# Kernel optimization log

Measured on AMD Instinct MI355X. Metric: run time of the kernel, lower is better.

## Reference

```python
import jax, jax.numpy as jnp
import numpy as np

B, T, C = 2, 2048, 1024
H = 4 * C           # MLP hidden (4*n_embd)
E_DYN = 7           # num_experts - static_experts
TOP_K = 2           # num_experts_per_tok
MOE_LOSS_COEF = 0.01


def setup_inputs() -> dict:
    key = jax.random.key(0)
    ks = jax.random.split(key, 6)
    s = 0.02
    x = jax.random.normal(ks[0], (B, T, C), dtype=jnp.float32)
    gate_w = jax.random.normal(ks[1], (C, E_DYN), dtype=jnp.float32) * s
    w1 = jax.random.normal(ks[2], (E_DYN, C, H), dtype=jnp.float32) * s   # dynamic experts c_fc
    w2 = jax.random.normal(ks[3], (E_DYN, H, C), dtype=jnp.float32) * s   # dynamic experts c_proj
    w1s = jax.random.normal(ks[4], (C, H), dtype=jnp.float32) * s         # static expert c_fc
    w2s = jax.random.normal(ks[5], (H, C), dtype=jnp.float32) * s         # static expert c_proj
    return {"x": x, "gate_w": gate_w, "w1": w1, "w2": w2, "w1s": w1s, "w2s": w2s}


def reference(x, gate_w, w1, w2, w1s, w2s):
    b, t, c = x.shape
    xf = x.reshape(-1, c)                                   # [N, C]
    n = xf.shape[0]

    # static expert (always applied)
    y_static = jax.nn.gelu(xf @ w1s, approximate=False) @ w2s  # [N, C]

    # gating: top-k + softmax over selected scores
    scores = xf @ gate_w                                    # [N, E]
    topk_scores, topk_idx = jax.lax.top_k(scores, TOP_K)    # [N, K]
    topk_w = jax.nn.softmax(topk_scores, axis=-1)           # [N, K]

    # dense dispatch weights [N, E] (top_k indices are distinct -> set is safe)
    probs = jnp.zeros((n, E_DYN), dtype=x.dtype)
    probs = probs.at[jnp.arange(n)[:, None], topk_idx].set(topk_w)

    # all-expert MLP then weighted combine (same math as masked per-expert dispatch)
    h = jax.nn.gelu(jnp.einsum('nc,ech->enh', xf, w1), approximate=False)  # [E, N, H]
    y_all = jnp.einsum('enh,ehc->enc', h, w2)               # [E, N, C]
    y_dyn = jnp.einsum('ne,enc->nc', probs, y_all)          # [N, C]

    y = (y_dyn + y_static).reshape(b, t, c)

    # variance_penalty auxiliary loss
    expert_usage = probs.mean(axis=0)                       # [E]
    variance = jnp.mean((expert_usage - expert_usage.mean()) ** 2)
    aux = MOE_LOSS_COEF * variance
    return y, aux
```

## Files before the change

kernel.cpp:

```cpp
#include <hip/hip_runtime.h>
#include <hip/hip_bf16.h>
#include <math.h>

#define N_TOK 4096
#define C_DIM 1024
#define H_DIM 4096
#define NEXP 7
#define NGRP 8
#define HCAP 13184

typedef __attribute__((ext_vector_type(8))) short short8;
typedef __attribute__((ext_vector_type(4))) float floatx4;

static const size_t OFF_COUNTS = 0;
static const size_t OFF_CURSOR = 64;
static const size_t OFF_BASE   = 128;
static const size_t OFF_PCOUNT = 192;
static const size_t OFF_CNT8   = 256;
static const size_t OFF_USAGE  = 320;
static const size_t OFF_TOPKI  = 4096;
static const size_t OFF_TOPKW  = OFF_TOPKI + 8192ull * 4;
static const size_t OFF_ETOK   = OFF_TOPKW + 8192ull * 4;
static const size_t OFF_EWT    = OFF_ETOK + (size_t)HCAP * 4;
static const size_t OFF_EIDX   = OFF_EWT + (size_t)HCAP * 4;
static const size_t OFF_XB     = 262144;
static const size_t OFF_W1T    = OFF_XB + (size_t)N_TOK * C_DIM * 2;
static const size_t OFF_W2T    = OFF_W1T + (size_t)NGRP * H_DIM * C_DIM * 2;
static const size_t OFF_H      = OFF_W2T + (size_t)NGRP * C_DIM * H_DIM * 2;

static __device__ __forceinline__ unsigned short f2bf(float f) {
    __hip_bfloat16 b = __float2bfloat16(f);
    return *reinterpret_cast<unsigned short*>(&b);
}
static __device__ __forceinline__ float bf2f(unsigned short u) {
    unsigned int v = ((unsigned int)u) << 16;
    return __builtin_bit_cast(float, v);
}

static __device__ __forceinline__ float gelu_f(float v) {
    float z = v * 0.70710678118654752f;
    float az = fabsf(z);
    float t = 1.0f / (1.0f + 0.3275911f * az);
    float poly = t * (0.254829592f + t * (-0.284496736f + t * (1.421413741f +
                 t * (-1.453152027f + t * 1.061405429f))));
    float erf_abs = 1.0f - poly * __expf(-az * az);
    float erf_v = (z < 0.f) ? -erf_abs : erf_abs;
    return 0.5f * v * (1.0f + erf_v);
}

static __device__ __forceinline__ void gll16(const void* g, void* l) {
    __builtin_amdgcn_global_load_lds((const __attribute__((address_space(1))) void*)g,
                                     (__attribute__((address_space(3))) void*)l, 16, 0, 0);
}

template <int VM> static __device__ __forceinline__ void wait_vm() {
    if constexpr (VM == 8) asm volatile("s_waitcnt vmcnt(8)" ::: "memory");
    else if constexpr (VM == 4) asm volatile("s_waitcnt vmcnt(4)" ::: "memory");
    else asm volatile("s_waitcnt vmcnt(0)" ::: "memory");
}
static __device__ __forceinline__ void barf() {
    __builtin_amdgcn_s_barrier();
    asm volatile("" ::: "memory");
}
static __device__ __forceinline__ void lgkm0_bar() {
    asm volatile("s_waitcnt lgkmcnt(0)" ::: "memory");
    __builtin_amdgcn_s_barrier();
    asm volatile("" ::: "memory");
}

static __device__ __forceinline__ void mfma_step(const char* Ap, const char* Bp,
    int wm, int wn, int l16, int rswz, floatx4 (&acc)[4][4])
{
    short8 a[4], b[4];
#pragma unroll
    for (int i = 0; i < 4; i++) {
        a[i] = *(const short8*)(Ap + ((wm * 64 + i * 16 + l16) * 64 + rswz));
        b[i] = *(const short8*)(Bp + ((wn * 64 + i * 16 + l16) * 64 + rswz));
    }
    __builtin_amdgcn_s_setprio(1);
#pragma unroll
    for (int i = 0; i < 4; i++)
#pragma unroll
        for (int j = 0; j < 4; j++)
            acc[i][j] = __builtin_amdgcn_mfma_f32_16x16x32_bf16(a[i], b[j], acc[i][j], 0, 0, 0);
    __builtin_amdgcn_s_setprio(0);
}

__global__ void init_small_kernel(int* counts, int* cursor, float* usage) {
    int i = threadIdx.x;
    if (i < 8) { counts[i] = 0; cursor[i] = 0; usage[i] = 0.f; }
}

__global__ void convert_x_kernel(const float* __restrict__ x, unsigned short* __restrict__ xb) {
    int i = blockIdx.x * 256 + threadIdx.x;
    float4 v = ((const float4*)x)[i];
    ushort4 o;
    o.x = f2bf(v.x); o.y = f2bf(v.y); o.z = f2bf(v.z); o.w = f2bf(v.w);
    ((ushort4*)xb)[i] = o;
}

__global__ __launch_bounds__(256) void transpose_cvt_kernel(
    const float* __restrict__ dyn, const float* __restrict__ stat,
    __hip_bfloat16* __restrict__ dst, int R, int S)
{
    int e = blockIdx.z;
    const float* src = (e < NEXP) ? (dyn + (size_t)e * R * S) : stat;
    unsigned short* d = (unsigned short*)(dst + (size_t)e * R * S);
    int s0 = blockIdx.x * 32, r0 = blockIdx.y * 64;
    __shared__ float t[64][33];
    int tx4 = threadIdx.x & 15, ty4 = threadIdx.x >> 4;
#pragma unroll
    for (int i = 0; i < 4; i++) {
        int r = ty4 + i * 16;
        float2 v = *(const float2*)(src + (size_t)(r0 + r) * S + s0 + tx4 * 2);
        t[r][tx4 * 2] = v.x; t[r][tx4 * 2 + 1] = v.y;
    }
    __syncthreads();
    int tx3 = threadIdx.x & 31, ty3 = threadIdx.x >> 5;
#pragma unroll
    for (int i = 0; i < 4; i++) {
        int s = ty3 + i * 8;
        int r = tx3 * 2;
        ushort2 o;
        o.x = f2bf(t[r][s]); o.y = f2bf(t[r + 1][s]);
        *(ushort2*)(d + (size_t)(s0 + s) * R + r0 + r) = o;
    }
}

__global__ __launch_bounds__(256) void gate_kernel(
    const float* __restrict__ x, const float* __restrict__ gw,
    int* __restrict__ topki, float* __restrict__ topkw,
    int* counts, float* usage)
{
    int wid = threadIdx.x >> 6, lane = threadIdx.x & 63;
    int t = blockIdx.x * 4 + wid;
    float s[NEXP];
#pragma unroll
    for (int e = 0; e < NEXP; e++) s[e] = 0.f;
    for (int c = lane; c < C_DIM; c += 64) {
        float xv = x[(size_t)t * C_DIM + c];
#pragma unroll
        for (int e = 0; e < NEXP; e++) s[e] += xv * gw[c * NEXP + e];
    }
#pragma unroll
    for (int e = 0; e < NEXP; e++)
        for (int off = 32; off > 0; off >>= 1) s[e] += __shfl_xor(s[e], off);
    if (lane == 0) {
        int e0 = 0;
        for (int e = 1; e < NEXP; e++) if (s[e] > s[e0]) e0 = e;
        int e1 = -1;
        for (int e = 0; e < NEXP; e++) {
            if (e == e0) continue;
            if (e1 < 0 || s[e] > s[e1]) e1 = e;
        }
        float w0 = 1.f / (1.f + expf(s[e1] - s[e0]));
        float w1 = 1.f - w0;
        topki[t * 2] = e0; topki[t * 2 + 1] = e1;
        topkw[t * 2] = w0; topkw[t * 2 + 1] = w1;
        atomicAdd(&counts[e0], 1); atomicAdd(&counts[e1], 1);
        atomicAdd(&usage[e0], w0); atomicAdd(&usage[e1], w1);
    }
}

__global__ __launch_bounds__(256) void prefix_kernel(
    const int* counts, const float* usage,
    int* base, int* pcount, int* cnt8,
    int* etok, float* ewt, float* y, int aux_index)
{
    __shared__ int sb[NGRP], sc[NGRP], sp[NGRP];
    if (threadIdx.x == 0) {
        int run = 0;
        for (int g = 0; g < NEXP; g++) {
            int c = counts[g];
            int p = (c + 127) & ~127;
            base[g] = run; pcount[g] = p; cnt8[g] = c;
            sb[g] = run; sc[g] = c; sp[g] = p;
            run += p;
        }
        base[NEXP] = run; pcount[NEXP] = N_TOK; cnt8[NEXP] = N_TOK;
        sb[NEXP] = run; sc[NEXP] = N_TOK; sp[NEXP] = N_TOK;
        float u[NEXP]; float mean = 0.f;
        for (int e = 0; e < NEXP; e++) { u[e] = usage[e] / (float)N_TOK; mean += u[e]; }
        mean /= (float)NEXP;
        float var = 0.f;
        for (int e = 0; e < NEXP; e++) { float dd = u[e] - mean; var += dd * dd; }
        var /= (float)NEXP;
        y[aux_index] = 0.01f * var;
    }
    __syncthreads();
    for (int i = threadIdx.x; i < N_TOK; i += 256) {
        etok[sb[NEXP] + i] = i; ewt[sb[NEXP] + i] = 1.0f;
    }
    for (int g = 0; g < NEXP; g++) {
        for (int i = sc[g] + (int)threadIdx.x; i < sp[g]; i += 256) {
            etok[sb[g] + i] = 0; ewt[sb[g] + i] = 0.f;
        }
    }
}

__global__ void scatter_kernel(const int* __restrict__ topki, const float* __restrict__ topkw,
                               const int* __restrict__ base, int* cursor,
                               int* __restrict__ etok, float* __restrict__ ewt,
                               int* __restrict__ eidx)
{
    int i = blockIdx.x * 256 + threadIdx.x;
    int t = i >> 1;
    int e = topki[i];
    float w = topkw[i];
    int pos = atomicAdd(&cursor[e], 1);
    int idx = base[e] + pos;
    etok[idx] = t; ewt[idx] = w;
    eidx[i] = idx;
}

__global__ __launch_bounds__(256) void gemm1_kernel(
    const __hip_bfloat16* __restrict__ xb,
    const __hip_bfloat16* __restrict__ w1t,
    __hip_bfloat16* __restrict__ h,
    const int* __restrict__ etok,
    const int* __restrict__ base,
    const int* __restrict__ pcount)
{
    int g = blockIdx.z, mt = blockIdx.y, ct = blockIdx.x;
    if (mt * 128 >= pcount[g]) return;
    int eb = base[g];

    __shared__ __align__(16) char Ab[3][8192];
    __shared__ __align__(16) char Bb[3][8192];

    int tid = threadIdx.x;
    int lane = tid & 63, wid = tid >> 6;
    int quad = lane >> 4, l16 = lane & 15;
    int wm = wid >> 1, wn = wid & 1;
    int rsub = lane >> 2, chunk = lane & 3;
    int swzc = chunk ^ ((rsub >> 1) & 3);
    int rswz = (quad ^ ((l16 >> 1) & 3)) * 16;

    const char* gA[2]; const char* gB[2]; int lo[2];
#pragma unroll
    for (int j = 0; j < 2; j++) {
        int row = wid * 32 + j * 16 + rsub;
        int tok = etok[eb + mt * 128 + row];
        gA[j] = (const char*)(xb + (size_t)tok * C_DIM) + swzc * 16;
        gB[j] = (const char*)(w1t + ((size_t)g * H_DIM + ct * 128 + row) * C_DIM) + swzc * 16;
        lo[j] = (wid * 32 + j * 16) * 64;
    }

#define STG(p, kt) do { size_t so = (size_t)(kt) * 64; \
        gll16(gA[0] + so, Ab[p] + lo[0]); \
        gll16(gA[1] + so, Ab[p] + lo[1]); \
        gll16(gB[0] + so, Bb[p] + lo[0]); \
        gll16(gB[1] + so, Bb[p] + lo[1]); } while (0)

    floatx4 acc[4][4] = {};
    const int nt = C_DIM / 32;
    STG(0, 0); STG(1, 1);
    int p = 0;
    for (int t = 0; t + 2 < nt; ++t) {
        int pn = p + 2; if (pn >= 3) pn -= 3;
        STG(pn, t + 2);
        wait_vm<8>();
        barf();
        mfma_step(Ab[p], Bb[p], wm, wn, l16, rswz, acc);
        lgkm0_bar();
        if (++p == 3) p = 0;
    }
    wait_vm<4>(); barf();
    mfma_step(Ab[0], Bb[0], wm, wn, l16, rswz, acc);
    lgkm0_bar();
    wait_vm<0>(); barf();
    mfma_step(Ab[1], Bb[1], wm, wn, l16, rswz, acc);
#undef STG

#pragma unroll
    for (int i = 0; i < 4; i++) {
        int rbase = mt * 128 + wm * 64 + i * 16 + quad * 4;
#pragma unroll
        for (int reg = 0; reg < 4; reg++) {
            size_t hrow = (size_t)(eb + rbase + reg) * H_DIM;
#pragma unroll
            for (int j = 0; j < 4; j++) {
                int cc = ct * 128 + wn * 64 + j * 16 + l16;
                h[hrow + cc] = __float2bfloat16(gelu_f(acc[i][j][reg]));
            }
        }
    }
}

__global__ __launch_bounds__(256) void gemm2_kernel(
    const __hip_bfloat16* __restrict__ h,
    const __hip_bfloat16* __restrict__ w2t,
    unsigned short* __restrict__ yp,
    const int* __restrict__ base,
    const int* __restrict__ pcount)
{
    int id = blockIdx.x;
    int xcd = id & 7;
    int jj  = id >> 3;
    int ct  = jj & 7;
    int g4  = xcd + ((jj >> 3) << 3);
    int mt  = g4 & 63, g = g4 >> 6;
    if (mt * 128 >= pcount[g]) return;
    int eb = base[g];

    __shared__ __align__(16) char Ab[3][8192];
    __shared__ __align__(16) char Bb[3][8192];

    int tid = threadIdx.x;
    int lane = tid & 63, wid = tid >> 6;
    int quad = lane >> 4, l16 = lane & 15;
    int wm = wid >> 1, wn = wid & 1;
    int rsub = lane >> 2, chunk = lane & 3;
    int swzc = chunk ^ ((rsub >> 1) & 3);
    int rswz = (quad ^ ((l16 >> 1) & 3)) * 16;

    const char* gA[2]; const char* gB[2]; int lo[2];
#pragma unroll
    for (int j = 0; j < 2; j++) {
        int row = wid * 32 + j * 16 + rsub;
        gA[j] = (const char*)(h + (size_t)(eb + mt * 128 + row) * H_DIM) + swzc * 16;
        gB[j] = (const char*)(w2t + ((size_t)g * C_DIM + ct * 128 + row) * H_DIM) + swzc * 16;
        lo[j] = (wid * 32 + j * 16) * 64;
    }

#define STG(p, kt) do { size_t so = (size_t)(kt) * 64; \
        gll16(gA[0] + so, Ab[p] + lo[0]); \
        gll16(gA[1] + so, Ab[p] + lo[1]); \
        gll16(gB[0] + so, Bb[p] + lo[0]); \
        gll16(gB[1] + so, Bb[p] + lo[1]); } while (0)

    floatx4 acc[4][4] = {};
    const int nt = H_DIM / 32;
    STG(0, 0); STG(1, 1);
    int p = 0;
    for (int t = 0; t + 2 < nt; ++t) {
        int pn = p + 2; if (pn >= 3) pn -= 3;
        STG(pn, t + 2);
        wait_vm<8>();
        barf();
        mfma_step(Ab[p], Bb[p], wm, wn, l16, rswz, acc);
        lgkm0_bar();
        if (++p == 3) p = 0;
    }
    wait_vm<4>(); barf();
    mfma_step(Ab[0], Bb[0], wm, wn, l16, rswz, acc);
    lgkm0_bar();
    wait_vm<0>(); barf();
    mfma_step(Ab[1], Bb[1], wm, wn, l16, rswz, acc);
#undef STG

#pragma unroll
    for (int i = 0; i < 4; i++) {
        int rl0 = mt * 128 + wm * 64 + i * 16 + quad * 4;
#pragma unroll
        for (int reg = 0; reg < 4; reg++) {
            size_t yrow = (size_t)(eb + rl0 + reg) * C_DIM;
#pragma unroll
            for (int j = 0; j < 4; j++) {
                int cc = ct * 128 + wn * 64 + j * 16 + l16;
                yp[yrow + cc] = f2bf(acc[i][j][reg]);
            }
        }
    }
}

__global__ __launch_bounds__(256) void combine_kernel(
    const unsigned short* __restrict__ yp,
    const int* __restrict__ eidx,
    const float* __restrict__ topkw,
    const int* __restrict__ base,
    float* __restrict__ y)
{
    int t = blockIdx.x;
    int i0 = eidx[t * 2], i1 = eidx[t * 2 + 1];
    float w0 = topkw[t * 2], w1 = topkw[t * 2 + 1];
    int is = base[NEXP] + t;
    int c = threadIdx.x * 4;
    ushort4 a = *(const ushort4*)(yp + (size_t)i0 * C_DIM + c);
    ushort4 b = *(const ushort4*)(yp + (size_t)i1 * C_DIM + c);
    ushort4 s = *(const ushort4*)(yp + (size_t)is * C_DIM + c);
    float4 o;
    o.x = w0 * bf2f(a.x) + w1 * bf2f(b.x) + bf2f(s.x);
    o.y = w0 * bf2f(a.y) + w1 * bf2f(b.y) + bf2f(s.y);
    o.z = w0 * bf2f(a.z) + w1 * bf2f(b.z) + bf2f(s.z);
    o.w = w0 * bf2f(a.w) + w1 * bf2f(b.w) + bf2f(s.w);
    *(float4*)(y + (size_t)t * C_DIM + c) = o;
}

extern "C" void kernel_launch(void* const* d_in, const int* in_sizes, int n_in,
                              void* d_out, int out_size, void* d_ws, size_t ws_size,
                              hipStream_t stream) {
    const float* x      = (const float*)d_in[0];
    const float* gate_w = (const float*)d_in[1];
    const float* w1     = (const float*)d_in[2];
    const float* w2     = (const float*)d_in[3];
    const float* w1s    = (const float*)d_in[4];
    const float* w2s    = (const float*)d_in[5];
    float* y = (float*)d_out;
    char* ws = (char*)d_ws;

    int*   counts = (int*)(ws + OFF_COUNTS);
    int*   cursor = (int*)(ws + OFF_CURSOR);
    int*   base   = (int*)(ws + OFF_BASE);
    int*   pcount = (int*)(ws + OFF_PCOUNT);
    int*   cnt8   = (int*)(ws + OFF_CNT8);
    float* usage  = (float*)(ws + OFF_USAGE);
    int*   topki  = (int*)(ws + OFF_TOPKI);
    float* topkw  = (float*)(ws + OFF_TOPKW);
    int*   etok   = (int*)(ws + OFF_ETOK);
    float* ewt    = (float*)(ws + OFF_EWT);
    int*   eidx   = (int*)(ws + OFF_EIDX);
    unsigned short* xb_u = (unsigned short*)(ws + OFF_XB);
    __hip_bfloat16* xb  = (__hip_bfloat16*)(ws + OFF_XB);
    __hip_bfloat16* w1t = (__hip_bfloat16*)(ws + OFF_W1T);
    __hip_bfloat16* w2t = (__hip_bfloat16*)(ws + OFF_W2T);
    __hip_bfloat16* hbuf = (__hip_bfloat16*)(ws + OFF_H);
    unsigned short* yp  = (unsigned short*)(ws + OFF_W1T);

    init_small_kernel<<<1, 64, 0, stream>>>(counts, cursor, usage);

    convert_x_kernel<<<(N_TOK * C_DIM / 4) / 256, 256, 0, stream>>>(x, xb_u);
    transpose_cvt_kernel<<<dim3(H_DIM / 32, C_DIM / 64, NGRP), 256, 0, stream>>>(w1, w1s, w1t, C_DIM, H_DIM);
    transpose_cvt_kernel<<<dim3(C_DIM / 32, H_DIM / 64, NGRP), 256, 0, stream>>>(w2, w2s, w2t, H_DIM, C_DIM);

    gate_kernel<<<N_TOK / 4, 256, 0, stream>>>(x, gate_w, topki, topkw, counts, usage);
    prefix_kernel<<<1, 256, 0, stream>>>(counts, usage, base, pcount, cnt8, etok, ewt, y, N_TOK * C_DIM);
    scatter_kernel<<<(N_TOK * 2) / 256, 256, 0, stream>>>(topki, topkw, base, cursor, etok, ewt, eidx);

    gemm1_kernel<<<dim3(H_DIM / 128, 64, NGRP), 256, 0, stream>>>(xb, w1t, hbuf, etok, base, pcount);
    gemm2_kernel<<<4096, 256, 0, stream>>>(hbuf, w2t, yp, base, pcount);
    combine_kernel<<<N_TOK, 256, 0, stream>>>(yp, eidx, topkw, base, y);
}
```

Baseline: 843.6 us.

## Enlarge grouped GEMM tiles to 256x256 with 8 waves and 4-stage LDS pipeline

Both expert GEMM kernels move from 128x128 tiles with 4 waves and triple buffering to 256x256 tiles with 8 waves, each wave computing a 128x64 sub-tile, plus a 4-deep global-to-LDS prefetch ring with a single barrier per K step. Block-to-tile mapping is redone so an XCD's blocks share expert and M-tile data across column tiles, and row guards are added for partial tiles. The aim is higher arithmetic intensity per LDS byte and fewer barriers. The cost is 128KB of LDS per block, more padding waste on per-expert row counts, and high register pressure from 32 accumulators per wave.

```diff
diff --git a/kernel.cpp b/kernel.cpp
--- a/kernel.cpp
+++ b/kernel.cpp
@@ -53,37 +53,12 @@
                                      (__attribute__((address_space(3))) void*)l, 16, 0, 0);
 }
 
-template <int VM> static __device__ __forceinline__ void wait_vm() {
-    if constexpr (VM == 8) asm volatile("s_waitcnt vmcnt(8)" ::: "memory");
-    else if constexpr (VM == 4) asm volatile("s_waitcnt vmcnt(4)" ::: "memory");
-    else asm volatile("s_waitcnt vmcnt(0)" ::: "memory");
-}
+static __device__ __forceinline__ void wait_vm8() { asm volatile("s_waitcnt vmcnt(8)" ::: "memory"); }
+static __device__ __forceinline__ void wait_vm4() { asm volatile("s_waitcnt vmcnt(4)" ::: "memory"); }
+static __device__ __forceinline__ void wait_vm0() { asm volatile("s_waitcnt vmcnt(0)" ::: "memory"); }
 static __device__ __forceinline__ void barf() {
     __builtin_amdgcn_s_barrier();
     asm volatile("" ::: "memory");
-}
-static __device__ __forceinline__ void lgkm0_bar() {
-    asm volatile("s_waitcnt lgkmcnt(0)" ::: "memory");
-    __builtin_amdgcn_s_barrier();
-    asm volatile("" ::: "memory");
-}
-
-static __device__ __forceinline__ void mfma_step(const char* Ap, const char* Bp,
-    int wm, int wn, int l16, int rswz, floatx4 (&acc)[4][4])
-{
-    short8 a[4], b[4];
-#pragma unroll
-    for (int i = 0; i < 4; i++) {
-        a[i] = *(const short8*)(Ap + ((wm * 64 + i * 16 + l16) * 64 + rswz));
-        b[i] = *(const short8*)(Bp + ((wn * 64 + i * 16 + l16) * 64 + rswz));
-    }
-    __builtin_amdgcn_s_setprio(1);
-#pragma unroll
-    for (int i = 0; i < 4; i++)
-#pragma unroll
-        for (int j = 0; j < 4; j++)
-            acc[i][j] = __builtin_amdgcn_mfma_f32_16x16x32_bf16(a[i], b[j], acc[i][j], 0, 0, 0);
-    __builtin_amdgcn_s_setprio(0);
 }
 
 __global__ void init_small_kernel(int* counts, int* cursor, float* usage) {
@@ -213,7 +188,14 @@
     eidx[i] = idx;
 }
 
-__global__ __launch_bounds__(256) void gemm1_kernel(
+
+#define STG1(T) do { int b_ = (T) & 3; size_t so_ = (size_t)(T) * 64; \
+        gll16(pA0 + so_, &Als[b_][w * 1024]); \
+        gll16(pA1 + so_, &Als[b_][8192 + w * 1024]); \
+        gll16(pB0 + so_, &Bls[b_][w * 1024]); \
+        gll16(pB1 + so_, &Bls[b_][8192 + w * 1024]); } while (0)
+
+__global__ __launch_bounds__(512, 2) void gemm1_kernel(
     const __hip_bfloat16* __restrict__ xb,
     const __hip_bfloat16* __restrict__ w1t,
     __hip_bfloat16* __restrict__ h,
@@ -221,73 +203,78 @@
     const int* __restrict__ base,
     const int* __restrict__ pcount)
 {
-    int g = blockIdx.z, mt = blockIdx.y, ct = blockIdx.x;
-    if (mt * 128 >= pcount[g]) return;
+    int id = blockIdx.x;
+    int xcd = id & 7, rest = id >> 3;
+    int ct = rest & 15, s = rest >> 4;
+    int g = s & 7;
+    int mt = ((xcd - g) & 7) + 8 * (s >> 3);
+    int psz = pcount[g];
+    if (mt * 256 >= psz) return;
     int eb = base[g];
 
-    __shared__ __align__(16) char Ab[3][8192];
-    __shared__ __align__(16) char Bb[3][8192];
-
-    int tid = threadIdx.x;
-    int lane = tid & 63, wid = tid >> 6;
+    __shared__ __align__(16) char Als[4][16384];
+    __shared__ __align__(16) char Bls[4][16384];
+
+    int tid = threadIdx.x, lane = tid & 63, w = tid >> 6;
+    int r0 = tid >> 2, c0 = tid & 3;
+    int cs = c0 ^ ((r0 >> 1) & 3);
+
+    int tokA0 = etok[eb + mt * 256 + r0];
+    int tokA1 = etok[eb + mt * 256 + 128 + r0];
+    const char* pA0 = (const char*)(xb + (size_t)tokA0 * C_DIM) + cs * 16;
+    const char* pA1 = (const char*)(xb + (size_t)tokA1 * C_DIM) + cs * 16;
+    const char* pB0 = (const char*)(w1t + ((size_t)g * H_DIM + ct * 256 + r0) * C_DIM) + cs * 16;
+    const char* pB1 = (const char*)(w1t + ((size_t)g * H_DIM + ct * 256 + 128 + r0) * C_DIM) + cs * 16;
+
+    int wm = w >> 2, wn = w & 3;
     int quad = lane >> 4, l16 = lane & 15;
-    int wm = wid >> 1, wn = wid & 1;
-    int rsub = lane >> 2, chunk = lane & 3;
-    int swzc = chunk ^ ((rsub >> 1) & 3);
     int rswz = (quad ^ ((l16 >> 1) & 3)) * 16;
 
-    const char* gA[2]; const char* gB[2]; int lo[2];
-#pragma unroll
-    for (int j = 0; j < 2; j++) {
-        int row = wid * 32 + j * 16 + rsub;
-        int tok = etok[eb + mt * 128 + row];
-        gA[j] = (const char*)(xb + (size_t)tok * C_DIM) + swzc * 16;
-        gB[j] = (const char*)(w1t + ((size_t)g * H_DIM + ct * 128 + row) * C_DIM) + swzc * 16;
-        lo[j] = (wid * 32 + j * 16) * 64;
-    }
-
-#define STG(p, kt) do { size_t so = (size_t)(kt) * 64; \
-        gll16(gA[0] + so, Ab[p] + lo[0]); \
-        gll16(gA[1] + so, Ab[p] + lo[1]); \
-        gll16(gB[0] + so, Bb[p] + lo[0]); \
-        gll16(gB[1] + so, Bb[p] + lo[1]); } while (0)
-
-    floatx4 acc[4][4] = {};
-    const int nt = C_DIM / 32;
-    STG(0, 0); STG(1, 1);
-    int p = 0;
-    for (int t = 0; t + 2 < nt; ++t) {
-        int pn = p + 2; if (pn >= 3) pn -= 3;
-        STG(pn, t + 2);
-        wait_vm<8>();
+    floatx4 acc[8][4] = {};
+    const int NT = C_DIM / 32;
+    STG1(0); STG1(1); STG1(2);
+    for (int T = 0; T < NT; ++T) {
+        int rem = NT - 1 - T;
+        if (rem >= 2) wait_vm8(); else if (rem == 1) wait_vm4(); else wait_vm0();
         barf();
-        mfma_step(Ab[p], Bb[p], wm, wn, l16, rswz, acc);
-        lgkm0_bar();
-        if (++p == 3) p = 0;
-    }
-    wait_vm<4>(); barf();
-    mfma_step(Ab[0], Bb[0], wm, wn, l16, rswz, acc);
-    lgkm0_bar();
-    wait_vm<0>(); barf();
-    mfma_step(Ab[1], Bb[1], wm, wn, l16, rswz, acc);
-#undef STG
-
-#pragma unroll
-    for (int i = 0; i < 4; i++) {
-        int rbase = mt * 128 + wm * 64 + i * 16 + quad * 4;
+        if (T + 3 < NT) STG1(T + 3);
+        const char* Ap = Als[T & 3];
+        const char* Bp = Bls[T & 3];
+        short8 a[8], b[4];
+#pragma unroll
+        for (int i = 0; i < 8; i++)
+            a[i] = *(const short8*)(Ap + (wm * 128 + i * 16 + l16) * 64 + rswz);
+#pragma unroll
+        for (int j = 0; j < 4; j++)
+            b[j] = *(const short8*)(Bp + (wn * 64 + j * 16 + l16) * 64 + rswz);
+        __builtin_amdgcn_s_setprio(1);
+#pragma unroll
+        for (int i = 0; i < 8; i++)
+#pragma unroll
+            for (int j = 0; j < 4; j++)
+                acc[i][j] = __builtin_amdgcn_mfma_f32_16x16x32_bf16(a[i], b[j], acc[i][j], 0, 0, 0);
+        __builtin_amdgcn_s_setprio(0);
+    }
+
+#pragma unroll
+    for (int i = 0; i < 8; i++) {
+        int lr0 = mt * 256 + wm * 128 + i * 16 + quad * 4;
 #pragma unroll
         for (int reg = 0; reg < 4; reg++) {
-            size_t hrow = (size_t)(eb + rbase + reg) * H_DIM;
-#pragma unroll
-            for (int j = 0; j < 4; j++) {
-                int cc = ct * 128 + wn * 64 + j * 16 + l16;
-                h[hrow + cc] = __float2bfloat16(gelu_f(acc[i][j][reg]));
+            int lr = lr0 + reg;
+            if (lr < psz) {
+                size_t hrow = (size_t)(eb + lr) * H_DIM;
+#pragma unroll
+                for (int j = 0; j < 4; j++) {
+                    int cc = ct * 256 + wn * 64 + j * 16 + l16;
+                    h[hrow + cc] = __float2bfloat16(gelu_f(acc[i][j][reg]));
+                }
             }
         }
     }
 }
 
-__global__ __launch_bounds__(256) void gemm2_kernel(
+__global__ __launch_bounds__(512, 2) void gemm2_kernel(
     const __hip_bfloat16* __restrict__ h,
     const __hip_bfloat16* __restrict__ w2t,
     unsigned short* __restrict__ yp,
@@ -295,70 +282,69 @@
     const int* __restrict__ pcount)
 {
     int id = blockIdx.x;
-    int xcd = id & 7;
-    int jj  = id >> 3;
-    int ct  = jj & 7;
-    int g4  = xcd + ((jj >> 3) << 3);
-    int mt  = g4 & 63, g = g4 >> 6;
-    if (mt * 128 >= pcount[g]) return;
+    int xcd = id & 7, rest = id >> 3;
+    int ct = rest & 3, s = rest >> 2;
+    int g = s & 7;
+    int mt = ((xcd - g) & 7) + 8 * (s >> 3);
+    int psz = pcount[g];
+    if (mt * 256 >= psz) return;
     int eb = base[g];
 
-    __shared__ __align__(16) char Ab[3][8192];
-    __shared__ __align__(16) char Bb[3][8192];
-
-    int tid = threadIdx.x;
-    int lane = tid & 63, wid = tid >> 6;
+    __shared__ __align__(16) char Als[4][16384];
+    __shared__ __align__(16) char Bls[4][16384];
+
+    int tid = threadIdx.x, lane = tid & 63, w = tid >> 6;
+    int r0 = tid >> 2, c0 = tid & 3;
+    int cs = c0 ^ ((r0 >> 1) & 3);
+
+    const char* pA0 = (const char*)(h + (size_t)(eb + mt * 256 + r0) * H_DIM) + cs * 16;
+    const char* pA1 = (const char*)(h + (size_t)(eb + mt * 256 + 128 + r0) * H_DIM) + cs * 16;
+    const char* pB0 = (const char*)(w2t + ((size_t)g * C_DIM + ct * 256 + r0) * H_DIM) + cs * 16;
+    const char* pB1 = (const char*)(w2t + ((size_t)g * C_DIM + ct * 256 + 128 + r0) * H_DIM) + cs * 16;
+
+    int wm = w >> 2, wn = w & 3;
     int quad = lane >> 4, l16 = lane & 15;
-    int wm = wid >> 1, wn = wid & 1;
-    int rsub = lane >> 2, chunk = lane & 3;
-    int swzc = chunk ^ ((rsub >> 1) & 3);
     int rswz = (quad ^ ((l16 >> 1) & 3)) * 16;
 
-    const char* gA[2]; const char* gB[2]; int lo[2];
-#pragma unroll
-    for (int j = 0; j < 2; j++) {
-        int row = wid * 32 + j * 16 + rsub;
-        gA[j] = (const char*)(h + (size_t)(eb + mt * 128 + row) * H_DIM) + swzc * 16;
-        gB[j] = (const char*)(w2t + ((size_t)g * C_DIM + ct * 128 + row) * H_DIM) + swzc * 16;
-        lo[j] = (wid * 32 + j * 16) * 64;
-    }
-
-#define STG(p, kt) do { size_t so = (size_t)(kt) * 64; \
-        gll16(gA[0] + so, Ab[p] + lo[0]); \
-        gll16(gA[1] + so, Ab[p] + lo[1]); \
-        gll16(gB[0] + so, Bb[p] + lo[0]); \
-        gll16(gB[1] + so, Bb[p] + lo[1]); } while (0)
-
-    floatx4 acc[4][4] = {};
-    const int nt = H_DIM / 32;
-    STG(0, 0); STG(1, 1);
-    int p = 0;
-    for (int t = 0; t + 2 < nt; ++t) {
-        int pn = p + 2; if (pn >= 3) pn -= 3;
-        STG(pn, t + 2);
-        wait_vm<8>();
+    floatx4 acc[8][4] = {};
+    const int NT = H_DIM / 32;
+    STG1(0); STG1(1); STG1(2);
+    for (int T = 0; T < NT; ++T) {
+        int rem = NT - 1 - T;
+        if (rem >= 2) wait_vm8(); else if (rem == 1) wait_vm4(); else wait_vm0();
         barf();
-        mfma_step(Ab[p], Bb[p], wm, wn, l16, rswz, acc);
-        lgkm0_bar();
-        if (++p == 3) p = 0;
-    }
-    wait_vm<4>(); barf();
-    mfma_step(Ab[0], Bb[0], wm, wn, l16, rswz, acc);
-    lgkm0_bar();
-    wait_vm<0>(); barf();
-    mfma_step(Ab[1], Bb[1], wm, wn, l16, rswz, acc);
-#undef STG
-
-#pragma unroll
-    for (int i = 0; i < 4; i++) {
-        int rl0 = mt * 128 + wm * 64 + i * 16 + quad * 4;
+        if (T + 3 < NT) STG1(T + 3);
+        const char* Ap = Als[T & 3];
+        const char* Bp = Bls[T & 3];
+        short8 a[8], b[4];
+#pragma unroll
+        for (int i = 0; i < 8; i++)
+            a[i] = *(const short8*)(Ap + (wm * 128 + i * 16 + l16) * 64 + rswz);
+#pragma unroll
+        for (int j = 0; j < 4; j++)
+            b[j] = *(const short8*)(Bp + (wn * 64 + j * 16 + l16) * 64 + rswz);
+        __builtin_amdgcn_s_setprio(1);
+#pragma unroll
+        for (int i = 0; i < 8; i++)
+#pragma unroll
+            for (int j = 0; j < 4; j++)
+                acc[i][j] = __builtin_amdgcn_mfma_f32_16x16x32_bf16(a[i], b[j], acc[i][j], 0, 0, 0);
+        __builtin_amdgcn_s_setprio(0);
+    }
+
+#pragma unroll
+    for (int i = 0; i < 8; i++) {
+        int lr0 = mt * 256 + wm * 128 + i * 16 + quad * 4;
 #pragma unroll
         for (int reg = 0; reg < 4; reg++) {
-            size_t yrow = (size_t)(eb + rl0 + reg) * C_DIM;
-#pragma unroll
-            for (int j = 0; j < 4; j++) {
-                int cc = ct * 128 + wn * 64 + j * 16 + l16;
-                yp[yrow + cc] = f2bf(acc[i][j][reg]);
+            int lr = lr0 + reg;
+            if (lr < psz) {
+                size_t yrow = (size_t)(eb + lr) * C_DIM;
+#pragma unroll
+                for (int j = 0; j < 4; j++) {
+                    int cc = ct * 256 + wn * 64 + j * 16 + l16;
+                    yp[yrow + cc] = f2bf(acc[i][j][reg]);
+                }
             }
         }
     }
@@ -427,7 +413,7 @@
     prefix_kernel<<<1, 256, 0, stream>>>(counts, usage, base, pcount, cnt8, etok, ewt, y, N_TOK * C_DIM);
     scatter_kernel<<<(N_TOK * 2) / 256, 256, 0, stream>>>(topki, topkw, base, cursor, etok, ewt, eidx);
 
-    gemm1_kernel<<<dim3(H_DIM / 128, 64, NGRP), 256, 0, stream>>>(xb, w1t, hbuf, etok, base, pcount);
-    gemm2_kernel<<<4096, 256, 0, stream>>>(hbuf, w2t, yp, base, pcount);
+    gemm1_kernel<<<4096, 512, 0, stream>>>(xb, w1t, hbuf, etok, base, pcount);
+    gemm2_kernel<<<1024, 512, 0, stream>>>(hbuf, w2t, yp, base, pcount);
     combine_kernel<<<N_TOK, 256, 0, stream>>>(yp, eidx, topkw, base, y);
 }
```

After: 856.6 us. No clear change (+1.5%).
